# Kernel optimization log

Hardware: AMD Instinct MI355X
Metric: run time of the kernel (lower is better)

## Reference

```python
import jax, jax.numpy as jnp
import numpy as np

H, B, T, DH = 16, 2, 2048, 64
MODEL_DIM = 1024


def setup_inputs() -> dict:
    key = jax.random.key(0)
    ks = jax.random.split(key, 5)
    q = jax.random.normal(ks[0], (H, B, T, DH), dtype=jnp.float32)
    k = jax.random.normal(ks[1], (H, B, T, DH), dtype=jnp.float32)
    v = jax.random.normal(ks[2], (H, B, T, DH), dtype=jnp.float32)
    Wo_w = jax.random.normal(ks[3], (MODEL_DIM, H * DH), dtype=jnp.float32) * 0.02
    Wo_b = jax.random.normal(ks[4], (MODEL_DIM,), dtype=jnp.float32) * 0.02
    return {"q": q, "k": k, "v": v, "Wo_w": Wo_w, "Wo_b": Wo_b}


def reference(q, k, v, Wo_w, Wo_b):
    # per-head scaled dot-product attention; scale uses per-head dk (=DH)
    scale = jnp.sqrt(jnp.asarray(DH, dtype=q.dtype))
    # scores: [H, B, T, T]
    scores = jnp.einsum('hbtd,hbsd->hbts', q, k) / scale
    # causal mask (additive -1e12 on strict upper triangle, matching torch code)
    mask = jnp.triu(jnp.ones((T, T), dtype=bool), 1)
    scores = scores + (-1e12) * mask.astype(scores.dtype)
    weights = jax.nn.softmax(scores, axis=-1)
    # context per head: [H, B, T, DH]
    context = jnp.einsum('hbts,hbsd->hbtd', weights, v)
    # concat heads along feature dim: [B, T, H*DH]
    context = jnp.transpose(context, (1, 2, 0, 3)).reshape(B, T, H * DH)
    # output projection (torch Linear: x @ W.T + b)
    return context @ Wo_w.T + Wo_b
```

## Files before the change

### kernel.cpp

```cpp
#include <hip/hip_runtime.h>

typedef __attribute__((ext_vector_type(8))) short bf16x8;
typedef __attribute__((ext_vector_type(4))) float f32x4;
typedef __attribute__((ext_vector_type(4))) unsigned int u32x4;
typedef __attribute__((ext_vector_type(4))) unsigned short u16x4;

#define H_ 16
#define B_ 2
#define T_ 2048
#define DH_ 64
#define MD_ 1024

static __device__ inline unsigned short f2bf(float f) {
    union { float f; unsigned u; } x; x.f = f;
    unsigned r = (x.u + 0x7fffu + ((x.u >> 16) & 1u)) >> 16;
    return (unsigned short)r;
}
static __device__ inline unsigned int pack_bf2(float lo, float hi) {
    return __builtin_amdgcn_perm(__float_as_uint(hi), __float_as_uint(lo), 0x07060302u);
}
static __device__ inline unsigned short hi16(float f) {
    return (unsigned short)(__float_as_uint(f) >> 16);
}

__global__ __launch_bounds__(256) void prep_k(const float* __restrict__ k,
                                              const float* __restrict__ v,
                                              const float* __restrict__ w,
                                              unsigned short* __restrict__ kb,
                                              unsigned short* __restrict__ vtb,
                                              unsigned short* __restrict__ wob) {
    __shared__ __attribute__((aligned(16))) unsigned short vt64[64][64];
    const int blk = blockIdx.x;
    const int tid = threadIdx.x;
    if (blk < 1024) {
        int i = (blk * 256 + tid) * 4;
        f32x4 x = *(const f32x4*)(w + i);
        u16x4 y;
        y[0] = f2bf(x[0]); y[1] = f2bf(x[1]); y[2] = f2bf(x[2]); y[3] = f2bf(x[3]);
        *(u16x4*)(wob + i) = y;
    } else if (blk < 2048) {
        int j = blk - 1024;
        const int hb = j >> 5, s0 = (j & 31) * 64;
        const int row = tid >> 2, c = (tid & 3) * 16;
        const long off = (long)hb * (T_ * DH_) + (long)(s0 + row) * DH_ + c;
        const float* p = k + off;
        f32x4 a0 = *(const f32x4*)p;
        f32x4 a1 = *(const f32x4*)(p + 4);
        f32x4 a2 = *(const f32x4*)(p + 8);
        f32x4 a3 = *(const f32x4*)(p + 12);
        u32x4 w0, w1;
        w0[0] = pack_bf2(a0[0], a0[1]); w0[1] = pack_bf2(a0[2], a0[3]);
        w0[2] = pack_bf2(a1[0], a1[1]); w0[3] = pack_bf2(a1[2], a1[3]);
        w1[0] = pack_bf2(a2[0], a2[1]); w1[1] = pack_bf2(a2[2], a2[3]);
        w1[2] = pack_bf2(a3[0], a3[1]); w1[3] = pack_bf2(a3[2], a3[3]);
        *(u32x4*)(kb + off) = w0;
        *(u32x4*)(kb + off + 8) = w1;
    } else {
        int j = blk - 2048;
        const int hb = j >> 5, s0 = (j & 31) * 64;
        const int vkp = tid & 31, vdg = tid >> 5;
        const float* vp = v + (long)hb * (T_ * DH_) + (long)(s0 + 2 * vkp) * DH_ + vdg * 8;
        f32x4 va0 = *(const f32x4*)vp;
        f32x4 va1 = *(const f32x4*)(vp + 4);
        f32x4 vb0 = *(const f32x4*)(vp + DH_);
        f32x4 vb1 = *(const f32x4*)(vp + DH_ + 4);
#pragma unroll
        for (int jj = 0; jj < 4; jj++) {
            ((unsigned int*)&vt64[vdg * 8 + jj][0])[vkp]     = pack_bf2(va0[jj], vb0[jj]);
            ((unsigned int*)&vt64[vdg * 8 + 4 + jj][0])[vkp] = pack_bf2(va1[jj], vb1[jj]);
        }
        __syncthreads();
        const int dh = tid >> 2, kc = (tid & 3) * 16;
        u32x4 o0 = *(const u32x4*)&vt64[dh][kc];
        u32x4 o1 = *(const u32x4*)&vt64[dh][kc + 8];
        unsigned short* op = vtb + (long)hb * (DH_ * T_) + (long)dh * T_ + s0 + kc;
        *(u32x4*)op = o0;
        *(u32x4*)(op + 8) = o1;
    }
}

__global__ __launch_bounds__(256, 4) void attn_k(const float* __restrict__ q,
                                                 const unsigned short* __restrict__ kb,
                                                 const unsigned short* __restrict__ vtb,
                                                 unsigned short* __restrict__ ctx) {
    const int i = blockIdx.x;
    const int xcd = i & 7, j = i >> 3;
    const int cu = j & 31, l = j >> 5;
    const int hb = xcd * 4 + l;
    const int t = (l & 1) ? (31 - cu) : cu;
    const int h = hb >> 1, b = hb & 1;
    const int tid = threadIdx.x;
    const int wave = tid >> 6, lane = tid & 63;
    const int ln = lane & 15, quad = lane >> 4;

    __shared__ __attribute__((aligned(16))) unsigned short kt[64][72];
    __shared__ __attribute__((aligned(16))) unsigned short vt[64][72];
    __shared__ __attribute__((aligned(16))) unsigned short pl[4][16][72];

    const long kbase = (long)hb * (T_ * DH_);
    const long vbase = (long)hb * (DH_ * T_);
    const int nsteps = t + 1;
    const int q0w = t * 64 + wave * 16;
    const int srow = tid >> 2, sc = (tid & 3) * 16;

    bf16x8 ones;
#pragma unroll
    for (int z = 0; z < 8; z++) ones[z] = (short)0x3F80;

    bf16x8 qf0, qf1;
    {
        const float* qp = q + kbase + (long)(q0w + ln) * DH_ + quad * 8;
        f32x4 a0 = *(const f32x4*)qp;
        f32x4 a1 = *(const f32x4*)(qp + 4);
        f32x4 b0 = *(const f32x4*)(qp + 32);
        f32x4 b1 = *(const f32x4*)(qp + 36);
#pragma unroll
        for (int z = 0; z < 4; z++) {
            qf0[z]   = (short)f2bf(a0[z] * 0.125f);
            qf0[4+z] = (short)f2bf(a1[z] * 0.125f);
            qf1[z]   = (short)f2bf(b0[z] * 0.125f);
            qf1[4+z] = (short)f2bf(b1[z] * 0.125f);
        }
    }

    f32x4 oacc[4];
#pragma unroll
    for (int z = 0; z < 4; z++) oacc[z] = f32x4{0.f, 0.f, 0.f, 0.f};
    f32x4 lacc = f32x4{0.f, 0.f, 0.f, 0.f};

    u32x4 kr0, kr1, vr0, vr1;
    {
        const unsigned short* kp = kb + kbase + (long)srow * DH_ + sc;
        kr0 = *(const u32x4*)kp; kr1 = *(const u32x4*)(kp + 8);
        const unsigned short* vp = vtb + vbase + (long)srow * T_ + sc;
        vr0 = *(const u32x4*)vp; vr1 = *(const u32x4*)(vp + 8);
    }

#pragma unroll 1
    for (int step = 0; step < nsteps; step++) {
        __syncthreads();
        *(u32x4*)&kt[srow][sc]     = kr0;
        *(u32x4*)&kt[srow][sc + 8] = kr1;
        *(u32x4*)&vt[srow][sc]     = vr0;
        *(u32x4*)&vt[srow][sc + 8] = vr1;
        __syncthreads();

        if (step + 1 < nsteps) {
            const unsigned short* kp = kb + kbase + (long)((step + 1) * 64 + srow) * DH_ + sc;
            kr0 = *(const u32x4*)kp; kr1 = *(const u32x4*)(kp + 8);
            const unsigned short* vp = vtb + vbase + (long)srow * T_ + (step + 1) * 64 + sc;
            vr0 = *(const u32x4*)vp; vr1 = *(const u32x4*)(vp + 8);
        }

        f32x4 sa[4];
#pragma unroll
        for (int nt = 0; nt < 4; nt++) {
            bf16x8 kf0 = *(const bf16x8*)&kt[nt * 16 + ln][quad * 8];
            bf16x8 kf1 = *(const bf16x8*)&kt[nt * 16 + ln][32 + quad * 8];
            f32x4 a = f32x4{0.f, 0.f, 0.f, 0.f};
            a = __builtin_amdgcn_mfma_f32_16x16x32_bf16(qf0, kf0, a, 0, 0, 0);
            a = __builtin_amdgcn_mfma_f32_16x16x32_bf16(qf1, kf1, a, 0, 0, 0);
            sa[nt] = a;
        }

        if (step == nsteps - 1) {
            const int lr = wave * 16 + quad * 4;
#pragma unroll
            for (int nt = 0; nt < 4; nt++)
#pragma unroll
                for (int r = 0; r < 4; r++) {
                    float p = __expf(sa[nt][r]);
                    if (nt * 16 + ln > lr + r) p = 0.f;
                    pl[wave][quad * 4 + r][nt * 16 + ln] = hi16(p);
                }
        } else {
#pragma unroll
            for (int nt = 0; nt < 4; nt++)
#pragma unroll
                for (int r = 0; r < 4; r++)
                    pl[wave][quad * 4 + r][nt * 16 + ln] = hi16(__expf(sa[nt][r]));
        }

        bf16x8 pf0 = *(const bf16x8*)&pl[wave][ln][quad * 8];
        bf16x8 pf1 = *(const bf16x8*)&pl[wave][ln][32 + quad * 8];

#pragma unroll
        for (int dt = 0; dt < 4; dt++) {
            bf16x8 vf0 = *(const bf16x8*)&vt[dt * 16 + ln][quad * 8];
            bf16x8 vf1 = *(const bf16x8*)&vt[dt * 16 + ln][32 + quad * 8];
            oacc[dt] = __builtin_amdgcn_mfma_f32_16x16x32_bf16(pf0, vf0, oacc[dt], 0, 0, 0);
            oacc[dt] = __builtin_amdgcn_mfma_f32_16x16x32_bf16(pf1, vf1, oacc[dt], 0, 0, 0);
        }
        lacc = __builtin_amdgcn_mfma_f32_16x16x32_bf16(pf0, ones, lacc, 0, 0, 0);
        lacc = __builtin_amdgcn_mfma_f32_16x16x32_bf16(pf1, ones, lacc, 0, 0, 0);
    }

#pragma unroll
    for (int r = 0; r < 4; r++) {
        float rl = __builtin_amdgcn_rcpf(lacc[r]);
        int row_g = q0w + quad * 4 + r;
#pragma unroll
        for (int dt = 0; dt < 4; dt++)
            ctx[(long)(b * T_ + row_g) * MD_ + h * 64 + dt * 16 + ln] =
                f2bf(oacc[dt][r] * rl);
    }
}

__global__ __launch_bounds__(256, 4) void proj_k(const unsigned short* __restrict__ A,
                                                 const unsigned short* __restrict__ Bw,
                                                 const float* __restrict__ bias,
                                                 float* __restrict__ out) {
    const int i = blockIdx.x;
    const int n0 = ((i & 7) * 2 + ((i >> 3) & 1)) * 64;
    const int m0 = (i >> 4) * 64;
    const int tid = threadIdx.x;
    const int wave = tid >> 6, lane = tid & 63;
    const int ln = lane & 15, quad = lane >> 4;

    __shared__ __attribute__((aligned(16))) unsigned short As[64][72];
    __shared__ __attribute__((aligned(16))) unsigned short Bs[64][72];

    const int srow = tid >> 2, sc = (tid & 3) * 16;

    f32x4 acc[4];
#pragma unroll
    for (int z = 0; z < 4; z++) acc[z] = f32x4{0.f, 0.f, 0.f, 0.f};

    u32x4 ar0, ar1, br0, br1;
    {
        const unsigned short* ap = A + (long)(m0 + srow) * 1024 + sc;
        ar0 = *(const u32x4*)ap; ar1 = *(const u32x4*)(ap + 8);
        const unsigned short* bp = Bw + (long)(n0 + srow) * 1024 + sc;
        br0 = *(const u32x4*)bp; br1 = *(const u32x4*)(bp + 8);
    }

#pragma unroll 1
    for (int ks = 0; ks < 1024; ks += 64) {
        __syncthreads();
        *(u32x4*)&As[srow][sc]     = ar0;
        *(u32x4*)&As[srow][sc + 8] = ar1;
        *(u32x4*)&Bs[srow][sc]     = br0;
        *(u32x4*)&Bs[srow][sc + 8] = br1;
        __syncthreads();

        if (ks + 64 < 1024) {
            const unsigned short* ap = A + (long)(m0 + srow) * 1024 + ks + 64 + sc;
            ar0 = *(const u32x4*)ap; ar1 = *(const u32x4*)(ap + 8);
            const unsigned short* bp = Bw + (long)(n0 + srow) * 1024 + ks + 64 + sc;
            br0 = *(const u32x4*)bp; br1 = *(const u32x4*)(bp + 8);
        }

        bf16x8 bf0 = *(const bf16x8*)&Bs[wave * 16 + ln][quad * 8];
        bf16x8 bf1 = *(const bf16x8*)&Bs[wave * 16 + ln][32 + quad * 8];
#pragma unroll
        for (int mt = 0; mt < 4; mt++) {
            bf16x8 af0 = *(const bf16x8*)&As[mt * 16 + ln][quad * 8];
            bf16x8 af1 = *(const bf16x8*)&As[mt * 16 + ln][32 + quad * 8];
            acc[mt] = __builtin_amdgcn_mfma_f32_16x16x32_bf16(af0, bf0, acc[mt], 0, 0, 0);
            acc[mt] = __builtin_amdgcn_mfma_f32_16x16x32_bf16(af1, bf1, acc[mt], 0, 0, 0);
        }
    }

    int col = n0 + wave * 16 + ln;
    float bz = bias[col];
#pragma unroll
    for (int mt = 0; mt < 4; mt++)
#pragma unroll
        for (int r = 0; r < 4; r++) {
            int row = m0 + mt * 16 + quad * 4 + r;
            out[(long)row * 1024 + col] = acc[mt][r] + bz;
        }
}

extern "C" void kernel_launch(void* const* d_in, const int* in_sizes, int n_in,
                              void* d_out, int out_size, void* d_ws, size_t ws_size,
                              hipStream_t stream) {
    const float* q    = (const float*)d_in[0];
    const float* k    = (const float*)d_in[1];
    const float* v    = (const float*)d_in[2];
    const float* Wo_w = (const float*)d_in[3];
    const float* Wo_b = (const float*)d_in[4];
    float* out = (float*)d_out;

    unsigned short* ctx = (unsigned short*)d_ws;
    unsigned short* wob = ctx + (size_t)4096 * 1024;
    unsigned short* kbb = wob + (size_t)1024 * 1024;
    unsigned short* vtb = kbb + (size_t)32 * 2048 * 64;

    prep_k<<<3072, 256, 0, stream>>>(k, v, Wo_w, kbb, vtb, wob);
    attn_k<<<1024, 256, 0, stream>>>(q, kbb, vtb, ctx);
    proj_k<<<1024, 256, 0, stream>>>(ctx, wob, Wo_b, out);
}
```

Measured before the change: 153.5 us.

## Split KV range across waves in attention; retile projection GEMM with 2x2 warp tiles

The attention kernel now uses 128-thread blocks, each covering 32 query rows, with the two waves splitting the key blocks between them (split-K style). K and V fragments are read directly from global memory instead of being staged in LDS, and partial O and row sums are merged through shared memory at the end. Tiles are ordered longest-first for load balance, and the diagonal block is half-skipped when it is fully masked. The projection GEMM moves to a 2x2 wave tiling with a 128-wide K step to improve fragment reuse and cut barriers. The cost is uncoalesced direct global fragment loads in attention and more registers per thread.

```diff
diff --git a/kernel.cpp b/kernel.cpp
--- a/kernel.cpp
+++ b/kernel.cpp
@@ -79,130 +79,145 @@
     }
 }
 
-__global__ __launch_bounds__(256, 4) void attn_k(const float* __restrict__ q,
+__global__ __launch_bounds__(128, 4) void attn_k(const float* __restrict__ q,
                                                  const unsigned short* __restrict__ kb,
                                                  const unsigned short* __restrict__ vtb,
                                                  unsigned short* __restrict__ ctx) {
-    const int i = blockIdx.x;
-    const int xcd = i & 7, j = i >> 3;
-    const int cu = j & 31, l = j >> 5;
-    const int hb = xcd * 4 + l;
-    const int t = (l & 1) ? (31 - cu) : cu;
+    const int bl = blockIdx.x;
+    const int xcd = bl & 7, s = bl >> 3;
+    const int hb = xcd * 4 + (s & 3);
+    const int qt = 63 - (s >> 2);
     const int h = hb >> 1, b = hb & 1;
     const int tid = threadIdx.x;
-    const int wave = tid >> 6, lane = tid & 63;
+    const int w = tid >> 6, lane = tid & 63;
     const int ln = lane & 15, quad = lane >> 4;
 
-    __shared__ __attribute__((aligned(16))) unsigned short kt[64][72];
-    __shared__ __attribute__((aligned(16))) unsigned short vt[64][72];
-    __shared__ __attribute__((aligned(16))) unsigned short pl[4][16][72];
+    __shared__ __attribute__((aligned(16))) unsigned short pl[2][32][72];
+    __shared__ __attribute__((aligned(16))) float po[32][64];
+    __shared__ float cl[32];
 
     const long kbase = (long)hb * (T_ * DH_);
     const long vbase = (long)hb * (DH_ * T_);
-    const int nsteps = t + 1;
-    const int q0w = t * 64 + wave * 16;
-    const int srow = tid >> 2, sc = (tid & 3) * 16;
+    const int nsteps = (qt >> 1) + 1;
+    const int qrow0 = qt * 32;
 
     bf16x8 ones;
 #pragma unroll
     for (int z = 0; z < 8; z++) ones[z] = (short)0x3F80;
 
-    bf16x8 qf0, qf1;
-    {
-        const float* qp = q + kbase + (long)(q0w + ln) * DH_ + quad * 8;
+    bf16x8 qf[2][2];
+#pragma unroll
+    for (int rf = 0; rf < 2; rf++) {
+        const float* qp = q + kbase + (long)(qrow0 + rf * 16 + ln) * DH_ + quad * 8;
         f32x4 a0 = *(const f32x4*)qp;
         f32x4 a1 = *(const f32x4*)(qp + 4);
         f32x4 b0 = *(const f32x4*)(qp + 32);
         f32x4 b1 = *(const f32x4*)(qp + 36);
 #pragma unroll
         for (int z = 0; z < 4; z++) {
-            qf0[z]   = (short)f2bf(a0[z] * 0.125f);
-            qf0[4+z] = (short)f2bf(a1[z] * 0.125f);
-            qf1[z]   = (short)f2bf(b0[z] * 0.125f);
-            qf1[4+z] = (short)f2bf(b1[z] * 0.125f);
-        }
-    }
-
-    f32x4 oacc[4];
-#pragma unroll
-    for (int z = 0; z < 4; z++) oacc[z] = f32x4{0.f, 0.f, 0.f, 0.f};
-    f32x4 lacc = f32x4{0.f, 0.f, 0.f, 0.f};
-
-    u32x4 kr0, kr1, vr0, vr1;
-    {
-        const unsigned short* kp = kb + kbase + (long)srow * DH_ + sc;
-        kr0 = *(const u32x4*)kp; kr1 = *(const u32x4*)(kp + 8);
-        const unsigned short* vp = vtb + vbase + (long)srow * T_ + sc;
-        vr0 = *(const u32x4*)vp; vr1 = *(const u32x4*)(vp + 8);
-    }
+            qf[rf][0][z]     = (short)f2bf(a0[z] * 0.125f);
+            qf[rf][0][4 + z] = (short)f2bf(a1[z] * 0.125f);
+            qf[rf][1][z]     = (short)f2bf(b0[z] * 0.125f);
+            qf[rf][1][4 + z] = (short)f2bf(b1[z] * 0.125f);
+        }
+    }
+
+    f32x4 oacc[2][4];
+#pragma unroll
+    for (int rf = 0; rf < 2; rf++)
+#pragma unroll
+        for (int dt = 0; dt < 4; dt++) oacc[rf][dt] = f32x4{0.f, 0.f, 0.f, 0.f};
+    f32x4 lacc[2];
+    lacc[0] = f32x4{0.f, 0.f, 0.f, 0.f};
+    lacc[1] = f32x4{0.f, 0.f, 0.f, 0.f};
 
 #pragma unroll 1
-    for (int step = 0; step < nsteps; step++) {
-        __syncthreads();
-        *(u32x4*)&kt[srow][sc]     = kr0;
-        *(u32x4*)&kt[srow][sc + 8] = kr1;
-        *(u32x4*)&vt[srow][sc]     = vr0;
-        *(u32x4*)&vt[srow][sc + 8] = vr1;
-        __syncthreads();
-
-        if (step + 1 < nsteps) {
-            const unsigned short* kp = kb + kbase + (long)((step + 1) * 64 + srow) * DH_ + sc;
-            kr0 = *(const u32x4*)kp; kr1 = *(const u32x4*)(kp + 8);
-            const unsigned short* vp = vtb + vbase + (long)srow * T_ + (step + 1) * 64 + sc;
-            vr0 = *(const u32x4*)vp; vr1 = *(const u32x4*)(vp + 8);
-        }
-
-        f32x4 sa[4];
+    for (int sg = w; sg < nsteps; sg += 2) {
+        const int s0 = sg * 64;
+        const bool last = (sg == nsteps - 1);
+        const bool halfstep = last && !(qt & 1);
+
 #pragma unroll
         for (int nt = 0; nt < 4; nt++) {
-            bf16x8 kf0 = *(const bf16x8*)&kt[nt * 16 + ln][quad * 8];
-            bf16x8 kf1 = *(const bf16x8*)&kt[nt * 16 + ln][32 + quad * 8];
-            f32x4 a = f32x4{0.f, 0.f, 0.f, 0.f};
-            a = __builtin_amdgcn_mfma_f32_16x16x32_bf16(qf0, kf0, a, 0, 0, 0);
-            a = __builtin_amdgcn_mfma_f32_16x16x32_bf16(qf1, kf1, a, 0, 0, 0);
-            sa[nt] = a;
-        }
-
-        if (step == nsteps - 1) {
-            const int lr = wave * 16 + quad * 4;
-#pragma unroll
-            for (int nt = 0; nt < 4; nt++)
+            if (halfstep && nt >= 2) continue;
+            const unsigned short* kp = kb + kbase + (long)(s0 + nt * 16 + ln) * DH_ + quad * 8;
+            bf16x8 kf0 = *(const bf16x8*)kp;
+            bf16x8 kf1 = *(const bf16x8*)(kp + 32);
+            f32x4 s0a = f32x4{0.f, 0.f, 0.f, 0.f};
+            f32x4 s1a = f32x4{0.f, 0.f, 0.f, 0.f};
+            s0a = __builtin_amdgcn_mfma_f32_16x16x32_bf16(qf[0][0], kf0, s0a, 0, 0, 0);
+            s0a = __builtin_amdgcn_mfma_f32_16x16x32_bf16(qf[0][1], kf1, s0a, 0, 0, 0);
+            s1a = __builtin_amdgcn_mfma_f32_16x16x32_bf16(qf[1][0], kf0, s1a, 0, 0, 0);
+            s1a = __builtin_amdgcn_mfma_f32_16x16x32_bf16(qf[1][1], kf1, s1a, 0, 0, 0);
+            const int colg = s0 + nt * 16 + ln;
+            if (last) {
 #pragma unroll
                 for (int r = 0; r < 4; r++) {
-                    float p = __expf(sa[nt][r]);
-                    if (nt * 16 + ln > lr + r) p = 0.f;
-                    pl[wave][quad * 4 + r][nt * 16 + ln] = hi16(p);
+                    float p0 = __expf(s0a[r]);
+                    if (colg > qrow0 + quad * 4 + r) p0 = 0.f;
+                    pl[w][quad * 4 + r][nt * 16 + ln] = hi16(p0);
+                    float p1 = __expf(s1a[r]);
+                    if (colg > qrow0 + 16 + quad * 4 + r) p1 = 0.f;
+                    pl[w][16 + quad * 4 + r][nt * 16 + ln] = hi16(p1);
                 }
-        } else {
-#pragma unroll
-            for (int nt = 0; nt < 4; nt++)
+            } else {
+#pragma unroll
+                for (int r = 0; r < 4; r++) {
+                    pl[w][quad * 4 + r][nt * 16 + ln]      = hi16(__expf(s0a[r]));
+                    pl[w][16 + quad * 4 + r][nt * 16 + ln] = hi16(__expf(s1a[r]));
+                }
+            }
+        }
+
+#pragma unroll
+        for (int hf = 0; hf < 2; hf++) {
+            if (halfstep && hf >= 1) continue;
+            bf16x8 pf0 = *(const bf16x8*)&pl[w][ln][hf * 32 + quad * 8];
+            bf16x8 pf1 = *(const bf16x8*)&pl[w][16 + ln][hf * 32 + quad * 8];
+            lacc[0] = __builtin_amdgcn_mfma_f32_16x16x32_bf16(pf0, ones, lacc[0], 0, 0, 0);
+            lacc[1] = __builtin_amdgcn_mfma_f32_16x16x32_bf16(pf1, ones, lacc[1], 0, 0, 0);
+#pragma unroll
+            for (int dt = 0; dt < 4; dt++) {
+                const unsigned short* vp = vtb + vbase + (long)(dt * 16 + ln) * T_ + s0 + hf * 32 + quad * 8;
+                bf16x8 vf = *(const bf16x8*)vp;
+                oacc[0][dt] = __builtin_amdgcn_mfma_f32_16x16x32_bf16(pf0, vf, oacc[0][dt], 0, 0, 0);
+                oacc[1][dt] = __builtin_amdgcn_mfma_f32_16x16x32_bf16(pf1, vf, oacc[1][dt], 0, 0, 0);
+            }
+        }
+    }
+
+    if (w == 1) {
+#pragma unroll
+        for (int rf = 0; rf < 2; rf++)
+#pragma unroll
+            for (int dt = 0; dt < 4; dt++)
 #pragma unroll
                 for (int r = 0; r < 4; r++)
-                    pl[wave][quad * 4 + r][nt * 16 + ln] = hi16(__expf(sa[nt][r]));
-        }
-
-        bf16x8 pf0 = *(const bf16x8*)&pl[wave][ln][quad * 8];
-        bf16x8 pf1 = *(const bf16x8*)&pl[wave][ln][32 + quad * 8];
-
-#pragma unroll
-        for (int dt = 0; dt < 4; dt++) {
-            bf16x8 vf0 = *(const bf16x8*)&vt[dt * 16 + ln][quad * 8];
-            bf16x8 vf1 = *(const bf16x8*)&vt[dt * 16 + ln][32 + quad * 8];
-            oacc[dt] = __builtin_amdgcn_mfma_f32_16x16x32_bf16(pf0, vf0, oacc[dt], 0, 0, 0);
-            oacc[dt] = __builtin_amdgcn_mfma_f32_16x16x32_bf16(pf1, vf1, oacc[dt], 0, 0, 0);
-        }
-        lacc = __builtin_amdgcn_mfma_f32_16x16x32_bf16(pf0, ones, lacc, 0, 0, 0);
-        lacc = __builtin_amdgcn_mfma_f32_16x16x32_bf16(pf1, ones, lacc, 0, 0, 0);
-    }
-
-#pragma unroll
-    for (int r = 0; r < 4; r++) {
-        float rl = __builtin_amdgcn_rcpf(lacc[r]);
-        int row_g = q0w + quad * 4 + r;
-#pragma unroll
-        for (int dt = 0; dt < 4; dt++)
-            ctx[(long)(b * T_ + row_g) * MD_ + h * 64 + dt * 16 + ln] =
-                f2bf(oacc[dt][r] * rl);
+                    po[rf * 16 + quad * 4 + r][dt * 16 + ln] = oacc[rf][dt][r];
+        if (ln == 0) {
+#pragma unroll
+            for (int rf = 0; rf < 2; rf++)
+#pragma unroll
+                for (int r = 0; r < 4; r++)
+                    cl[rf * 16 + quad * 4 + r] = lacc[rf][r];
+        }
+    }
+    __syncthreads();
+    if (w == 0) {
+        unsigned short* cp = ctx + (long)(b * T_ + qrow0) * MD_ + h * 64;
+#pragma unroll
+        for (int rf = 0; rf < 2; rf++)
+#pragma unroll
+            for (int r = 0; r < 4; r++) {
+                const int row = rf * 16 + quad * 4 + r;
+                float l = lacc[rf][r] + cl[row];
+                float rl = __builtin_amdgcn_rcpf(l);
+#pragma unroll
+                for (int dt = 0; dt < 4; dt++) {
+                    float o = oacc[rf][dt][r] + po[row][dt * 16 + ln];
+                    cp[(long)row * MD_ + dt * 16 + ln] = f2bf(o * rl);
+                }
+            }
     }
 }
 
@@ -215,61 +230,76 @@
     const int m0 = (i >> 4) * 64;
     const int tid = threadIdx.x;
     const int wave = tid >> 6, lane = tid & 63;
+    const int wm = wave >> 1, wn = wave & 1;
     const int ln = lane & 15, quad = lane >> 4;
 
-    __shared__ __attribute__((aligned(16))) unsigned short As[64][72];
-    __shared__ __attribute__((aligned(16))) unsigned short Bs[64][72];
-
-    const int srow = tid >> 2, sc = (tid & 3) * 16;
-
-    f32x4 acc[4];
-#pragma unroll
-    for (int z = 0; z < 4; z++) acc[z] = f32x4{0.f, 0.f, 0.f, 0.f};
-
-    u32x4 ar0, ar1, br0, br1;
+    __shared__ __attribute__((aligned(16))) unsigned short As[64][136];
+    __shared__ __attribute__((aligned(16))) unsigned short Bs[64][136];
+
+    const int srow = tid >> 2, sc = (tid & 3) * 32;
+
+    f32x4 acc[2][2];
+#pragma unroll
+    for (int a = 0; a < 2; a++)
+#pragma unroll
+        for (int c = 0; c < 2; c++) acc[a][c] = f32x4{0.f, 0.f, 0.f, 0.f};
+
+    u32x4 ar[4], br[4];
     {
         const unsigned short* ap = A + (long)(m0 + srow) * 1024 + sc;
-        ar0 = *(const u32x4*)ap; ar1 = *(const u32x4*)(ap + 8);
         const unsigned short* bp = Bw + (long)(n0 + srow) * 1024 + sc;
-        br0 = *(const u32x4*)bp; br1 = *(const u32x4*)(bp + 8);
+#pragma unroll
+        for (int z = 0; z < 4; z++) {
+            ar[z] = *(const u32x4*)(ap + z * 8);
+            br[z] = *(const u32x4*)(bp + z * 8);
+        }
     }
 
 #pragma unroll 1
-    for (int ks = 0; ks < 1024; ks += 64) {
+    for (int ks = 0; ks < 1024; ks += 128) {
         __syncthreads();
-        *(u32x4*)&As[srow][sc]     = ar0;
-        *(u32x4*)&As[srow][sc + 8] = ar1;
-        *(u32x4*)&Bs[srow][sc]     = br0;
-        *(u32x4*)&Bs[srow][sc + 8] = br1;
+#pragma unroll
+        for (int z = 0; z < 4; z++) {
+            *(u32x4*)&As[srow][sc + z * 8] = ar[z];
+            *(u32x4*)&Bs[srow][sc + z * 8] = br[z];
+        }
         __syncthreads();
 
-        if (ks + 64 < 1024) {
-            const unsigned short* ap = A + (long)(m0 + srow) * 1024 + ks + 64 + sc;
-            ar0 = *(const u32x4*)ap; ar1 = *(const u32x4*)(ap + 8);
-            const unsigned short* bp = Bw + (long)(n0 + srow) * 1024 + ks + 64 + sc;
-            br0 = *(const u32x4*)bp; br1 = *(const u32x4*)(bp + 8);
-        }
-
-        bf16x8 bf0 = *(const bf16x8*)&Bs[wave * 16 + ln][quad * 8];
-        bf16x8 bf1 = *(const bf16x8*)&Bs[wave * 16 + ln][32 + quad * 8];
-#pragma unroll
-        for (int mt = 0; mt < 4; mt++) {
-            bf16x8 af0 = *(const bf16x8*)&As[mt * 16 + ln][quad * 8];
-            bf16x8 af1 = *(const bf16x8*)&As[mt * 16 + ln][32 + quad * 8];
-            acc[mt] = __builtin_amdgcn_mfma_f32_16x16x32_bf16(af0, bf0, acc[mt], 0, 0, 0);
-            acc[mt] = __builtin_amdgcn_mfma_f32_16x16x32_bf16(af1, bf1, acc[mt], 0, 0, 0);
-        }
-    }
-
-    int col = n0 + wave * 16 + ln;
-    float bz = bias[col];
-#pragma unroll
-    for (int mt = 0; mt < 4; mt++)
-#pragma unroll
-        for (int r = 0; r < 4; r++) {
-            int row = m0 + mt * 16 + quad * 4 + r;
-            out[(long)row * 1024 + col] = acc[mt][r] + bz;
-        }
+        if (ks + 128 < 1024) {
+            const unsigned short* ap = A + (long)(m0 + srow) * 1024 + ks + 128 + sc;
+            const unsigned short* bp = Bw + (long)(n0 + srow) * 1024 + ks + 128 + sc;
+#pragma unroll
+            for (int z = 0; z < 4; z++) {
+                ar[z] = *(const u32x4*)(ap + z * 8);
+                br[z] = *(const u32x4*)(bp + z * 8);
+            }
+        }
+
+#pragma unroll
+        for (int kk = 0; kk < 4; kk++) {
+            bf16x8 af0 = *(const bf16x8*)&As[wm * 32 + ln][kk * 32 + quad * 8];
+            bf16x8 af1 = *(const bf16x8*)&As[wm * 32 + 16 + ln][kk * 32 + quad * 8];
+            bf16x8 bf0 = *(const bf16x8*)&Bs[wn * 32 + ln][kk * 32 + quad * 8];
+            bf16x8 bf1 = *(const bf16x8*)&Bs[wn * 32 + 16 + ln][kk * 32 + quad * 8];
+            acc[0][0] = __builtin_amdgcn_mfma_f32_16x16x32_bf16(af0, bf0, acc[0][0], 0, 0, 0);
+            acc[0][1] = __builtin_amdgcn_mfma_f32_16x16x32_bf16(af0, bf1, acc[0][1], 0, 0, 0);
+            acc[1][0] = __builtin_amdgcn_mfma_f32_16x16x32_bf16(af1, bf0, acc[1][0], 0, 0, 0);
+            acc[1][1] = __builtin_amdgcn_mfma_f32_16x16x32_bf16(af1, bf1, acc[1][1], 0, 0, 0);
+        }
+    }
+
+#pragma unroll
+    for (int nt = 0; nt < 2; nt++) {
+        int col = n0 + wn * 32 + nt * 16 + ln;
+        float bz = bias[col];
+#pragma unroll
+        for (int mt = 0; mt < 2; mt++)
+#pragma unroll
+            for (int r = 0; r < 4; r++) {
+                int row = m0 + wm * 32 + mt * 16 + quad * 4 + r;
+                out[(long)row * 1024 + col] = acc[mt][nt][r] + bz;
+            }
+    }
 }
 
 extern "C" void kernel_launch(void* const* d_in, const int* in_sizes, int n_in,
@@ -288,6 +318,6 @@
     unsigned short* vtb = kbb + (size_t)32 * 2048 * 64;
 
     prep_k<<<3072, 256, 0, stream>>>(k, v, Wo_w, kbb, vtb, wob);
-    attn_k<<<1024, 256, 0, stream>>>(q, kbb, vtb, ctx);
+    attn_k<<<2048, 128, 0, stream>>>(q, kbb, vtb, ctx);
     proj_k<<<1024, 256, 0, stream>>>(ctx, wob, Wo_b, out);
 }
```

New measurement: 189.5 us. 1.23x slower.

## Split attention KV range in two and merge partials inside projection GEMM

Applied to the files above, without the earlier changes.

Each query tile's key range is now split across two blocks (even/odd KV tiles), doubling the grid and ordering blocks longest-first to improve load balance across CUs. Unnormalized partial outputs and row sums are written to a workspace, and the projection kernel merges the two partials, normalizes, and converts to bf16 while staging A into shared memory. The projection also switches to a 2x2 wave tiling with K-step 128, and the attention kernel's launch bound occupancy hint is raised. This trades extra global traffic for the doubled partial buffers against better parallelism on the causal triangle. Skipping the max-subtraction relies on bounded scores, which the code before already did.

```diff
diff --git a/kernel.cpp b/kernel.cpp
--- a/kernel.cpp
+++ b/kernel.cpp
@@ -79,16 +79,15 @@
     }
 }
 
-__global__ __launch_bounds__(256, 4) void attn_k(const float* __restrict__ q,
+__global__ __launch_bounds__(256, 5) void attn_k(const float* __restrict__ q,
                                                  const unsigned short* __restrict__ kb,
                                                  const unsigned short* __restrict__ vtb,
-                                                 unsigned short* __restrict__ ctx) {
-    const int i = blockIdx.x;
-    const int xcd = i & 7, j = i >> 3;
-    const int cu = j & 31, l = j >> 5;
-    const int hb = xcd * 4 + l;
-    const int t = (l & 1) ? (31 - cu) : cu;
-    const int h = hb >> 1, b = hb & 1;
+                                                 unsigned short* __restrict__ pbuf,
+                                                 float* __restrict__ lbuf) {
+    const int bl = blockIdx.x;
+    const int t = 31 - (bl >> 6);
+    const int inner = bl & 63;
+    const int hb = inner >> 1, j = inner & 1;
     const int tid = threadIdx.x;
     const int wave = tid >> 6, lane = tid & 63;
     const int ln = lane & 15, quad = lane >> 4;
@@ -129,15 +128,16 @@
     f32x4 lacc = f32x4{0.f, 0.f, 0.f, 0.f};
 
     u32x4 kr0, kr1, vr0, vr1;
-    {
-        const unsigned short* kp = kb + kbase + (long)srow * DH_ + sc;
+    if (j < nsteps) {
+        const unsigned short* kp = kb + kbase + (long)(j * 64 + srow) * DH_ + sc;
         kr0 = *(const u32x4*)kp; kr1 = *(const u32x4*)(kp + 8);
-        const unsigned short* vp = vtb + vbase + (long)srow * T_ + sc;
+        const unsigned short* vp = vtb + vbase + (long)srow * T_ + j * 64 + sc;
         vr0 = *(const u32x4*)vp; vr1 = *(const u32x4*)(vp + 8);
     }
 
 #pragma unroll 1
-    for (int step = 0; step < nsteps; step++) {
+    for (int sg = j; sg < nsteps; sg += 2) {
+        const int s0 = sg * 64;
         __syncthreads();
         *(u32x4*)&kt[srow][sc]     = kr0;
         *(u32x4*)&kt[srow][sc + 8] = kr1;
@@ -145,10 +145,10 @@
         *(u32x4*)&vt[srow][sc + 8] = vr1;
         __syncthreads();
 
-        if (step + 1 < nsteps) {
-            const unsigned short* kp = kb + kbase + (long)((step + 1) * 64 + srow) * DH_ + sc;
+        if (sg + 2 < nsteps) {
+            const unsigned short* kp = kb + kbase + (long)((sg + 2) * 64 + srow) * DH_ + sc;
             kr0 = *(const u32x4*)kp; kr1 = *(const u32x4*)(kp + 8);
-            const unsigned short* vp = vtb + vbase + (long)srow * T_ + (step + 1) * 64 + sc;
+            const unsigned short* vp = vtb + vbase + (long)srow * T_ + (sg + 2) * 64 + sc;
             vr0 = *(const u32x4*)vp; vr1 = *(const u32x4*)(vp + 8);
         }
 
@@ -163,7 +163,7 @@
             sa[nt] = a;
         }
 
-        if (step == nsteps - 1) {
+        if (sg == nsteps - 1) {
             const int lr = wave * 16 + quad * 4;
 #pragma unroll
             for (int nt = 0; nt < 4; nt++)
@@ -195,18 +195,24 @@
         lacc = __builtin_amdgcn_mfma_f32_16x16x32_bf16(pf1, ones, lacc, 0, 0, 0);
     }
 
+    const int jb = (hb * 32 + t) * 2 + j;
+    unsigned short* op = pbuf + (long)jb * 4096;
 #pragma unroll
     for (int r = 0; r < 4; r++) {
-        float rl = __builtin_amdgcn_rcpf(lacc[r]);
-        int row_g = q0w + quad * 4 + r;
+        const int row = wave * 16 + quad * 4 + r;
 #pragma unroll
         for (int dt = 0; dt < 4; dt++)
-            ctx[(long)(b * T_ + row_g) * MD_ + h * 64 + dt * 16 + ln] =
-                f2bf(oacc[dt][r] * rl);
-    }
-}
-
-__global__ __launch_bounds__(256, 4) void proj_k(const unsigned short* __restrict__ A,
+            op[row * 64 + dt * 16 + ln] = f2bf(oacc[dt][r]);
+    }
+    if (ln == 0) {
+#pragma unroll
+        for (int r = 0; r < 4; r++)
+            lbuf[jb * 64 + wave * 16 + quad * 4 + r] = lacc[r];
+    }
+}
+
+__global__ __launch_bounds__(256, 4) void proj_k(const unsigned short* __restrict__ pbuf,
+                                                 const float* __restrict__ lbuf,
                                                  const unsigned short* __restrict__ Bw,
                                                  const float* __restrict__ bias,
                                                  float* __restrict__ out) {
@@ -215,61 +221,102 @@
     const int m0 = (i >> 4) * 64;
     const int tid = threadIdx.x;
     const int wave = tid >> 6, lane = tid & 63;
+    const int wm = wave >> 1, wn = wave & 1;
     const int ln = lane & 15, quad = lane >> 4;
 
-    __shared__ __attribute__((aligned(16))) unsigned short As[64][72];
-    __shared__ __attribute__((aligned(16))) unsigned short Bs[64][72];
-
-    const int srow = tid >> 2, sc = (tid & 3) * 16;
-
-    f32x4 acc[4];
-#pragma unroll
-    for (int z = 0; z < 4; z++) acc[z] = f32x4{0.f, 0.f, 0.f, 0.f};
-
-    u32x4 ar0, ar1, br0, br1;
+    __shared__ __attribute__((aligned(16))) unsigned short As[64][136];
+    __shared__ __attribute__((aligned(16))) unsigned short Bs[64][136];
+
+    const int srow = tid >> 2, sc = (tid & 3) * 32;
+    const int m = m0 + srow;
+    const int b = m >> 11, tt = m & 2047;
+    const int tile = tt >> 6, r64 = tt & 63;
+
+    f32x4 acc[2][2];
+#pragma unroll
+    for (int a = 0; a < 2; a++)
+#pragma unroll
+        for (int c = 0; c < 2; c++) acc[a][c] = f32x4{0.f, 0.f, 0.f, 0.f};
+
+    u32x4 p0r[4], p1r[4], br[4];
+    float lsum;
     {
-        const unsigned short* ap = A + (long)(m0 + srow) * 1024 + sc;
-        ar0 = *(const u32x4*)ap; ar1 = *(const u32x4*)(ap + 8);
+        const int hh = sc >> 6;
+        const int hb = hh * 2 + b;
+        const long base = ((long)(hb * 32 + tile) * 2) * 4096 + r64 * 64 + (sc & 63);
+#pragma unroll
+        for (int z = 0; z < 4; z++) {
+            p0r[z] = *(const u32x4*)(pbuf + base + z * 8);
+            p1r[z] = *(const u32x4*)(pbuf + base + 4096 + z * 8);
+        }
+        lsum = lbuf[(hb * 32 + tile) * 128 + r64] + lbuf[(hb * 32 + tile) * 128 + 64 + r64];
         const unsigned short* bp = Bw + (long)(n0 + srow) * 1024 + sc;
-        br0 = *(const u32x4*)bp; br1 = *(const u32x4*)(bp + 8);
+#pragma unroll
+        for (int z = 0; z < 4; z++) br[z] = *(const u32x4*)(bp + z * 8);
     }
 
 #pragma unroll 1
-    for (int ks = 0; ks < 1024; ks += 64) {
-        __syncthreads();
-        *(u32x4*)&As[srow][sc]     = ar0;
-        *(u32x4*)&As[srow][sc + 8] = ar1;
-        *(u32x4*)&Bs[srow][sc]     = br0;
-        *(u32x4*)&Bs[srow][sc + 8] = br1;
-        __syncthreads();
-
-        if (ks + 64 < 1024) {
-            const unsigned short* ap = A + (long)(m0 + srow) * 1024 + ks + 64 + sc;
-            ar0 = *(const u32x4*)ap; ar1 = *(const u32x4*)(ap + 8);
-            const unsigned short* bp = Bw + (long)(n0 + srow) * 1024 + ks + 64 + sc;
-            br0 = *(const u32x4*)bp; br1 = *(const u32x4*)(bp + 8);
-        }
-
-        bf16x8 bf0 = *(const bf16x8*)&Bs[wave * 16 + ln][quad * 8];
-        bf16x8 bf1 = *(const bf16x8*)&Bs[wave * 16 + ln][32 + quad * 8];
-#pragma unroll
-        for (int mt = 0; mt < 4; mt++) {
-            bf16x8 af0 = *(const bf16x8*)&As[mt * 16 + ln][quad * 8];
-            bf16x8 af1 = *(const bf16x8*)&As[mt * 16 + ln][32 + quad * 8];
-            acc[mt] = __builtin_amdgcn_mfma_f32_16x16x32_bf16(af0, bf0, acc[mt], 0, 0, 0);
-            acc[mt] = __builtin_amdgcn_mfma_f32_16x16x32_bf16(af1, bf1, acc[mt], 0, 0, 0);
-        }
-    }
-
-    int col = n0 + wave * 16 + ln;
-    float bz = bias[col];
-#pragma unroll
-    for (int mt = 0; mt < 4; mt++)
-#pragma unroll
-        for (int r = 0; r < 4; r++) {
-            int row = m0 + mt * 16 + quad * 4 + r;
-            out[(long)row * 1024 + col] = acc[mt][r] + bz;
-        }
+    for (int ks = 0; ks < 1024; ks += 128) {
+        __syncthreads();
+        {
+            const float rl = __builtin_amdgcn_rcpf(lsum);
+#pragma unroll
+            for (int z = 0; z < 4; z++) {
+                u32x4 c;
+#pragma unroll
+                for (int w = 0; w < 4; w++) {
+                    unsigned a0 = p0r[z][w], a1 = p1r[z][w];
+                    float lo = __uint_as_float(a0 << 16) + __uint_as_float(a1 << 16);
+                    float hi = __uint_as_float(a0 & 0xffff0000u) + __uint_as_float(a1 & 0xffff0000u);
+                    c[w] = pack_bf2(lo * rl, hi * rl);
+                }
+                *(u32x4*)&As[srow][sc + z * 8] = c;
+                *(u32x4*)&Bs[srow][sc + z * 8] = br[z];
+            }
+        }
+        __syncthreads();
+
+        if (ks + 128 < 1024) {
+            const int kc = ks + 128 + sc;
+            const int hh = kc >> 6;
+            const int hb = hh * 2 + b;
+            const long base = ((long)(hb * 32 + tile) * 2) * 4096 + r64 * 64 + (kc & 63);
+#pragma unroll
+            for (int z = 0; z < 4; z++) {
+                p0r[z] = *(const u32x4*)(pbuf + base + z * 8);
+                p1r[z] = *(const u32x4*)(pbuf + base + 4096 + z * 8);
+            }
+            lsum = lbuf[(hb * 32 + tile) * 128 + r64] + lbuf[(hb * 32 + tile) * 128 + 64 + r64];
+            const unsigned short* bp = Bw + (long)(n0 + srow) * 1024 + ks + 128 + sc;
+#pragma unroll
+            for (int z = 0; z < 4; z++) br[z] = *(const u32x4*)(bp + z * 8);
+        }
+
+#pragma unroll
+        for (int kk = 0; kk < 4; kk++) {
+            bf16x8 af0 = *(const bf16x8*)&As[wm * 32 + ln][kk * 32 + quad * 8];
+            bf16x8 af1 = *(const bf16x8*)&As[wm * 32 + 16 + ln][kk * 32 + quad * 8];
+            bf16x8 bf0 = *(const bf16x8*)&Bs[wn * 32 + ln][kk * 32 + quad * 8];
+            bf16x8 bf1 = *(const bf16x8*)&Bs[wn * 32 + 16 + ln][kk * 32 + quad * 8];
+            acc[0][0] = __builtin_amdgcn_mfma_f32_16x16x32_bf16(af0, bf0, acc[0][0], 0, 0, 0);
+            acc[0][1] = __builtin_amdgcn_mfma_f32_16x16x32_bf16(af0, bf1, acc[0][1], 0, 0, 0);
+            acc[1][0] = __builtin_amdgcn_mfma_f32_16x16x32_bf16(af1, bf0, acc[1][0], 0, 0, 0);
+            acc[1][1] = __builtin_amdgcn_mfma_f32_16x16x32_bf16(af1, bf1, acc[1][1], 0, 0, 0);
+        }
+    }
+
+#pragma unroll
+    for (int nt = 0; nt < 2; nt++) {
+        int col = n0 + wn * 32 + nt * 16 + ln;
+        float bz = bias[col];
+#pragma unroll
+        for (int mt = 0; mt < 2; mt++)
+#pragma unroll
+            for (int r = 0; r < 4; r++) {
+                int row = m0 + wm * 32 + mt * 16 + quad * 4 + r;
+                out[(long)row * 1024 + col] = acc[mt][nt][r] + bz;
+            }
+    }
 }
 
 extern "C" void kernel_launch(void* const* d_in, const int* in_sizes, int n_in,
@@ -282,12 +329,13 @@
     const float* Wo_b = (const float*)d_in[4];
     float* out = (float*)d_out;
 
-    unsigned short* ctx = (unsigned short*)d_ws;
-    unsigned short* wob = ctx + (size_t)4096 * 1024;
-    unsigned short* kbb = wob + (size_t)1024 * 1024;
-    unsigned short* vtb = kbb + (size_t)32 * 2048 * 64;
+    unsigned short* wob  = (unsigned short*)d_ws;
+    unsigned short* kbb  = wob + (size_t)1024 * 1024;
+    unsigned short* vtb  = kbb + (size_t)32 * 2048 * 64;
+    unsigned short* pbuf = vtb + (size_t)32 * 64 * 2048;
+    float*          lbuf = (float*)(pbuf + (size_t)2048 * 4096);
 
     prep_k<<<3072, 256, 0, stream>>>(k, v, Wo_w, kbb, vtb, wob);
-    attn_k<<<1024, 256, 0, stream>>>(q, kbb, vtb, ctx);
-    proj_k<<<1024, 256, 0, stream>>>(ctx, wob, Wo_b, out);
-}
+    attn_k<<<2048, 256, 0, stream>>>(q, kbb, vtb, pbuf, lbuf);
+    proj_k<<<1024, 256, 0, stream>>>(pbuf, lbuf, wob, Wo_b, out);
+}
```

Result: slower. 165.3 us (+7.7%).
